# Kernel tuning notes

Hardware: AMD Instinct MI355X
Metric: run time of the kernel (lower is better)

## Reference

```python
import jax, jax.numpy as jnp
import numpy as np

DIM = 512  # module's self.dim, used for the softmax scale (note: NOT head dim)

def setup_inputs() -> dict:
    key = jax.random.key(0)
    kq, kk, kv = jax.random.split(key, 3)
    shape = (4, 8, 2048, 64)  # [B, H, S, Dh]
    q = jax.random.normal(kq, shape, dtype=jnp.float32)
    k = jax.random.normal(kk, shape, dtype=jnp.float32)
    v = jax.random.normal(kv, shape, dtype=jnp.float32)
    return {"q": q, "k": k, "v": v, "n": 2048}

def reference(q, k, v, n):
    # scores = q @ k^T, then divide by sqrt(dim) AFTER matmul (as in source)
    scores = jnp.einsum('bhqd,bhkd->bhqk', q, k)
    scale = jnp.sqrt(jnp.asarray(DIM, dtype=scores.dtype))
    p_attn = jax.nn.softmax(scores / scale, axis=-1)
    return jnp.einsum('bhqk,bhkd->bhqd', p_attn, v)
```

## Files before the change

### kernel.cpp

```cpp
#include <hip/hip_runtime.h>


using half8   = __attribute__((ext_vector_type(8))) _Float16;
using half4   = __attribute__((ext_vector_type(4))) _Float16;
using half2v  = __attribute__((ext_vector_type(2))) _Float16;
using f32x4   = __attribute__((ext_vector_type(4))) float;
using f32x16  = __attribute__((ext_vector_type(16))) float;
using int4v   = __attribute__((ext_vector_type(4))) int;

static __device__ __forceinline__ half2v cvt_pk(float a, float b) {
    return __builtin_bit_cast(half2v, __builtin_amdgcn_cvt_pkrtz(a, b));
}
static __device__ __forceinline__ int cvt_pk_i(float a, float b) {
    return __builtin_bit_cast(int, __builtin_amdgcn_cvt_pkrtz(a, b));
}

#define SEQ   2048
#define DH    64
#define QB    128
#define KVB   64
#define NKVT  (SEQ / KVB)
#define NQB   (SEQ / QB)
#define NBH   32
#define TILE_IMG_BYTES 16384
#define QSCALE (1.4426950408889634f / 22.627416997969522f)

#if __has_builtin(__builtin_amdgcn_exp2f)
#define EXP2F __builtin_amdgcn_exp2f
#else
#define EXP2F exp2f
#endif

#define GLOFF(dst, base, IMM)                                              \
    asm volatile("global_load_dwordx4 %0, %1, off offset:" #IMM            \
                 : "=v"(dst) : "v"(base) : "memory")

#define WAIT_VM(N)                                             \
    do {                                                       \
        asm volatile("s_waitcnt vmcnt(" #N ")" ::: "memory");  \
        __builtin_amdgcn_sched_barrier(0);                     \
    } while (0)

#define PLSWAP(a, b) \
    asm volatile("s_nop 1\n\tv_permlane32_swap_b32 %0, %1" : "+v"(a), "+v"(b))

#define MFMA32(A, B, C) __builtin_amdgcn_mfma_f32_32x32x16_f16((A), (B), (C), 0, 0, 0)

static __device__ __forceinline__ f32x16 z16() {
    f32x16 v;
#pragma unroll
    for (int i = 0; i < 16; ++i) v[i] = 0.f;
    return v;
}

#define ISSUE_K(KB, kvt)                                                   \
    do {                                                                   \
        const char* b0_ = imgbase + (size_t)(kvt) * TILE_IMG_BYTES + lane * 16; \
        GLOFF((KB)[0], b0_, 0);    GLOFF((KB)[1], b0_, 1024);              \
        GLOFF((KB)[2], b0_, 2048); GLOFF((KB)[3], b0_, 3072);              \
        const char* b1_ = b0_ + 4096;                                      \
        GLOFF((KB)[4], b1_, 0);    GLOFF((KB)[5], b1_, 1024);              \
        GLOFF((KB)[6], b1_, 2048); GLOFF((KB)[7], b1_, 3072);              \
    } while (0)

#define ISSUE_V(VB, kvt)                                                   \
    do {                                                                   \
        const char* b0_ = imgbase + (size_t)(kvt) * TILE_IMG_BYTES + 8192 + lane * 16; \
        GLOFF((VB)[0], b0_, 0);    GLOFF((VB)[1], b0_, 1024);              \
        GLOFF((VB)[2], b0_, 2048); GLOFF((VB)[3], b0_, 3072);              \
        const char* b1_ = b0_ + 4096;                                      \
        GLOFF((VB)[4], b1_, 0);    GLOFF((VB)[5], b1_, 1024);              \
        GLOFF((VB)[6], b1_, 2048); GLOFF((VB)[7], b1_, 3072);              \
    } while (0)

#define QK_TILE(KB, ST0, ST1)                                              \
    do {                                                                   \
        __builtin_amdgcn_s_setprio(1);                                     \
        _Pragma("unroll")                                                  \
        for (int ks = 0; ks < 4; ++ks) {                                   \
            (ST0) = MFMA32((KB)[ks],     qfrag[ks], (ST0));                \
            (ST1) = MFMA32((KB)[4 + ks], qfrag[ks], (ST1));                \
        }                                                                  \
        __builtin_amdgcn_s_setprio(0);                                     \
    } while (0)

#define SOFTPACK(ST0, ST1, PA)                                            \
    do {                                                                  \
        _Pragma("unroll")                                                 \
        for (int kvs2 = 0; kvs2 < 2; ++kvs2) {                            \
            const f32x16& st_ = kvs2 ? (ST1) : (ST0);                     \
            float p[16];                                                  \
            _Pragma("unroll")                                             \
            for (int r = 0; r < 16; ++r) p[r] = EXP2F(st_[r]);            \
            float s0 = 0.f, s1 = 0.f;                                     \
            _Pragma("unroll")                                             \
            for (int r = 0; r < 8; ++r) { s0 += p[r]; s1 += p[r + 8]; }   \
            lsum += s0 + s1;                                              \
            int m0 = cvt_pk_i(p[0],  p[1]),  m1 = cvt_pk_i(p[2],  p[3]);  \
            int m2 = cvt_pk_i(p[4],  p[5]),  m3 = cvt_pk_i(p[6],  p[7]);  \
            int m4 = cvt_pk_i(p[8],  p[9]),  m5 = cvt_pk_i(p[10], p[11]); \
            int m6 = cvt_pk_i(p[12], p[13]), m7 = cvt_pk_i(p[14], p[15]); \
            PLSWAP(m0, m2); PLSWAP(m1, m3);                               \
            PLSWAP(m4, m6); PLSWAP(m5, m7);                               \
            int4v t0; t0[0] = m0; t0[1] = m1; t0[2] = m2; t0[3] = m3;     \
            int4v t1; t1[0] = m4; t1[1] = m5; t1[2] = m6; t1[3] = m7;     \
            (PA)[2 * kvs2 + 0] = __builtin_bit_cast(half8, t0);           \
            (PA)[2 * kvs2 + 1] = __builtin_bit_cast(half8, t1);           \
        }                                                                 \
    } while (0)

#define PV_TILE(PA, VB)                                                    \
    do {                                                                   \
        __builtin_amdgcn_s_setprio(1);                                     \
        _Pragma("unroll")                                                  \
        for (int ks = 0; ks < 4; ++ks) {                                   \
            acc0 = MFMA32((PA)[ks], (VB)[ks],     acc0);                   \
            acc1 = MFMA32((PA)[ks], (VB)[4 + ks], acc1);                   \
        }                                                                  \
        __builtin_amdgcn_s_setprio(0);                                     \
    } while (0)

__global__ __launch_bounds__(256)
void prep_kv(const float* __restrict__ Kg, const float* __restrict__ Vg,
             char* __restrict__ ws)
{
    __shared__ __align__(16) _Float16 Kl[64][72];
    __shared__ __align__(16) _Float16 Vt[64][72];

    const int bid = blockIdx.x;
    const int bh  = bid >> 5;
    const int kvt = bid & 31;
    const int tid = threadIdx.x;

    const float* kg = Kg + ((size_t)bh * SEQ + (size_t)kvt * 64) * DH;
    const float* vg = Vg + ((size_t)bh * SEQ + (size_t)kvt * 64) * DH;
#pragma unroll
    for (int rr = 0; rr < 4; ++rr) {
        int row = rr * 16 + (tid >> 4);
        int c4  = (tid & 15) * 4;
        f32x4 kk = *(const f32x4*)(kg + (size_t)row * DH + c4);
        f32x4 vv = *(const f32x4*)(vg + (size_t)row * DH + c4);
#pragma unroll
        for (int j = 0; j < 4; ++j) {
            Kl[row][c4 + j] = (_Float16)kk[j];
            Vt[c4 + j][row] = (_Float16)vv[j];
        }
    }
    __syncthreads();

    char* out = ws + (size_t)bid * TILE_IMG_BYTES;
#pragma unroll
    for (int rep = 0; rep < 2; ++rep) {
        int f    = rep * 256 + tid;
        int ln   = f & 63;
        int ks   = (f >> 6) & 3;
        int g2   = f >> 8;
        int row  = g2 * 32 + (ln & 31);
        int colh = ks * 16 + (ln >> 5) * 8;
        *(half8*)(out + f * 16)        = *(const half8*)&Kl[row][colh];
        *(half8*)(out + 8192 + f * 16) = *(const half8*)&Vt[row][colh];
    }
}

__global__ __launch_bounds__(256, 2)
void fattn_fwd(const float* __restrict__ Qg, const char* __restrict__ Wimg,
               float* __restrict__ Og)
{
    const int tid  = threadIdx.x;
    const int lane = tid & 63;
    const int wave = tid >> 6;
    const int l31  = lane & 31;
    const int hi   = lane >> 5;

    const int wg  = blockIdx.x;
    const int swz = (wg & 7) * 64 + (wg >> 3);
    const int qb  = swz & (NQB - 1);
    const int bh  = swz >> 4;
    const size_t base = (size_t)bh * (SEQ * DH);

    half8 qfrag[4];
    {
        const int qrow = qb * QB + wave * 32 + l31;
        const float* qp = Qg + base + (size_t)qrow * DH + hi * 8;
#pragma unroll
        for (int ks = 0; ks < 4; ++ks) {
            f32x4 a = *(const f32x4*)(qp + ks * 16);
            f32x4 b = *(const f32x4*)(qp + ks * 16 + 4);
            half8 f;
#pragma unroll
            for (int i = 0; i < 4; ++i) f[i]     = (_Float16)(a[i] * QSCALE);
#pragma unroll
            for (int i = 0; i < 4; ++i) f[i + 4] = (_Float16)(b[i] * QSCALE);
            qfrag[ks] = f;
        }
    }

    f32x16 acc0 = z16(), acc1 = z16();
    float lsum = 0.f;

    const char* imgbase = Wimg + (size_t)(bh * NKVT) * TILE_IMG_BYTES;

    half8 kE[8], kO[8], vv[8];

    ISSUE_K(kE, 0);
    ISSUE_V(vv, 0);

#pragma unroll 1
    for (int t = 0; t < NKVT; t += 2) {
        WAIT_VM(8);
        f32x16 st0 = z16(), st1 = z16();
        QK_TILE(kE, st0, st1);
        ISSUE_K(kO, t + 1);
        half8 PA[4];
        SOFTPACK(st0, st1, PA);
        WAIT_VM(8);
        PV_TILE(PA, vv);
        ISSUE_V(vv, t + 1);

        WAIT_VM(8);
        f32x16 su0 = z16(), su1 = z16();
        QK_TILE(kO, su0, su1);
        if (t + 2 < NKVT) ISSUE_K(kE, t + 2);
        half8 PB[4];
        SOFTPACK(su0, su1, PB);
        if (t + 2 < NKVT) { WAIT_VM(8); } else { WAIT_VM(0); }
        PV_TILE(PB, vv);
        if (t + 2 < NKVT) ISSUE_V(vv, t + 2);
    }

    lsum += __shfl_xor(lsum, 32);
    const float invl = 1.f / lsum;
    const int qstrip = qb * QB + wave * 32;
#pragma unroll
    for (int r = 0; r < 16; ++r) {
        int q16 = (r & 3) + 8 * (r >> 2) + 4 * hi;
        float sc = __shfl(invl, q16);
        float* op = Og + base + (size_t)(qstrip + q16) * DH;
        op[l31]      = acc0[r] * sc;
        op[32 + l31] = acc1[r] * sc;
    }
}

extern "C" void kernel_launch(void* const* d_in, const int* in_sizes, int n_in,
                              void* d_out, int out_size, void* d_ws, size_t ws_size,
                              hipStream_t stream) {
    const float* q = (const float*)d_in[0];
    const float* k = (const float*)d_in[1];
    const float* v = (const float*)d_in[2];
    float* o = (float*)d_out;
    char* ws = (char*)d_ws;
    prep_kv<<<dim3(NBH * NKVT, 1, 1), dim3(256, 1, 1), 0, stream>>>(k, v, ws);
    fattn_fwd<<<dim3(NQB * NBH, 1, 1), dim3(256, 1, 1), 0, stream>>>(q, ws, o);
}
```

Baseline: 63.83 us.

## Stage KV tiles through shared memory via direct global-to-LDS loads

Instead of every wave loading the full K and V tile images from global memory into registers, the four waves cooperatively copy each 16KB tile into a double-buffered LDS array using global_load_lds, then each wave reads its fragments from LDS. This cuts redundant global/L2 traffic by a factor of the wave count and frees registers. In exchange it adds a workgroup barrier per KV tile, LDS read latency, and a shallower prefetch (one tile ahead, unrolled by one instead of two).

```diff
diff --git a/kernel.cpp b/kernel.cpp
--- a/kernel.cpp
+++ b/kernel.cpp
@@ -31,9 +31,10 @@
 #define EXP2F exp2f
 #endif
 
-#define GLOFF(dst, base, IMM)                                              \
-    asm volatile("global_load_dwordx4 %0, %1, off offset:" #IMM            \
-                 : "=v"(dst) : "v"(base) : "memory")
+#define GLDS(gp, lp)                                                      \
+    __builtin_amdgcn_global_load_lds(                                     \
+        (const __attribute__((address_space(1))) void*)(gp),              \
+        (__attribute__((address_space(3))) void*)(lp), 16, 0, 0)
 
 #define WAIT_VM(N)                                             \
     do {                                                       \
@@ -41,6 +42,12 @@
         __builtin_amdgcn_sched_barrier(0);                     \
     } while (0)
 
+#define WAIT_LGKM(N)                                           \
+    do {                                                       \
+        asm volatile("s_waitcnt lgkmcnt(" #N ")" ::: "memory");\
+        __builtin_amdgcn_sched_barrier(0);                     \
+    } while (0)
+
 #define PLSWAP(a, b) \
     asm volatile("s_nop 1\n\tv_permlane32_swap_b32 %0, %1" : "+v"(a), "+v"(b))
 
@@ -52,37 +59,6 @@
     for (int i = 0; i < 16; ++i) v[i] = 0.f;
     return v;
 }
-
-#define ISSUE_K(KB, kvt)                                                   \
-    do {                                                                   \
-        const char* b0_ = imgbase + (size_t)(kvt) * TILE_IMG_BYTES + lane * 16; \
-        GLOFF((KB)[0], b0_, 0);    GLOFF((KB)[1], b0_, 1024);              \
-        GLOFF((KB)[2], b0_, 2048); GLOFF((KB)[3], b0_, 3072);              \
-        const char* b1_ = b0_ + 4096;                                      \
-        GLOFF((KB)[4], b1_, 0);    GLOFF((KB)[5], b1_, 1024);              \
-        GLOFF((KB)[6], b1_, 2048); GLOFF((KB)[7], b1_, 3072);              \
-    } while (0)
-
-#define ISSUE_V(VB, kvt)                                                   \
-    do {                                                                   \
-        const char* b0_ = imgbase + (size_t)(kvt) * TILE_IMG_BYTES + 8192 + lane * 16; \
-        GLOFF((VB)[0], b0_, 0);    GLOFF((VB)[1], b0_, 1024);              \
-        GLOFF((VB)[2], b0_, 2048); GLOFF((VB)[3], b0_, 3072);              \
-        const char* b1_ = b0_ + 4096;                                      \
-        GLOFF((VB)[4], b1_, 0);    GLOFF((VB)[5], b1_, 1024);              \
-        GLOFF((VB)[6], b1_, 2048); GLOFF((VB)[7], b1_, 3072);              \
-    } while (0)
-
-#define QK_TILE(KB, ST0, ST1)                                              \
-    do {                                                                   \
-        __builtin_amdgcn_s_setprio(1);                                     \
-        _Pragma("unroll")                                                  \
-        for (int ks = 0; ks < 4; ++ks) {                                   \
-            (ST0) = MFMA32((KB)[ks],     qfrag[ks], (ST0));                \
-            (ST1) = MFMA32((KB)[4 + ks], qfrag[ks], (ST1));                \
-        }                                                                  \
-        __builtin_amdgcn_s_setprio(0);                                     \
-    } while (0)
 
 #define SOFTPACK(ST0, ST1, PA)                                            \
     do {                                                                  \
@@ -109,17 +85,6 @@
         }                                                                 \
     } while (0)
 
-#define PV_TILE(PA, VB)                                                    \
-    do {                                                                   \
-        __builtin_amdgcn_s_setprio(1);                                     \
-        _Pragma("unroll")                                                  \
-        for (int ks = 0; ks < 4; ++ks) {                                   \
-            acc0 = MFMA32((PA)[ks], (VB)[ks],     acc0);                   \
-            acc1 = MFMA32((PA)[ks], (VB)[4 + ks], acc1);                   \
-        }                                                                  \
-        __builtin_amdgcn_s_setprio(0);                                     \
-    } while (0)
-
 __global__ __launch_bounds__(256)
 void prep_kv(const float* __restrict__ Kg, const float* __restrict__ Vg,
              char* __restrict__ ws)
@@ -166,6 +131,8 @@
 void fattn_fwd(const float* __restrict__ Qg, const char* __restrict__ Wimg,
                float* __restrict__ Og)
 {
+    __shared__ __align__(16) char KVl[2][TILE_IMG_BYTES];
+
     const int tid  = threadIdx.x;
     const int lane = tid & 63;
     const int wave = tid >> 6;
@@ -199,33 +166,63 @@
     float lsum = 0.f;
 
     const char* imgbase = Wimg + (size_t)(bh * NKVT) * TILE_IMG_BYTES;
-
-    half8 kE[8], kO[8], vv[8];
-
-    ISSUE_K(kE, 0);
-    ISSUE_V(vv, 0);
+    const int sfrag = wave * 4;
+
+    auto stage = [&](int kvt, int b) {
+        const char* g = imgbase + (size_t)kvt * TILE_IMG_BYTES
+                        + sfrag * 1024 + lane * 16;
+        char* l = &KVl[b][sfrag * 1024];
+        GLDS(g,        l);
+        GLDS(g + 1024, l + 1024);
+        GLDS(g + 2048, l + 2048);
+        GLDS(g + 3072, l + 3072);
+    };
+
+    stage(0, 0);
 
 #pragma unroll 1
-    for (int t = 0; t < NKVT; t += 2) {
-        WAIT_VM(8);
+    for (int t = 0; t < NKVT; ++t) {
+        const int cur = t & 1;
+
+        WAIT_VM(0);
+        __builtin_amdgcn_s_barrier();
+        if (t + 1 < NKVT) stage(t + 1, cur ^ 1);
+
+        const char* kb = KVl[cur];
+
+        half8 kf[8];
+#pragma unroll
+        for (int j = 0; j < 8; ++j)
+            kf[j] = *(const half8*)(kb + j * 1024 + lane * 16);
+        __builtin_amdgcn_sched_barrier(0);
+        half8 vf[8];
+#pragma unroll
+        for (int j = 0; j < 8; ++j)
+            vf[j] = *(const half8*)(kb + 8192 + j * 1024 + lane * 16);
+
+        WAIT_LGKM(8);
+
         f32x16 st0 = z16(), st1 = z16();
-        QK_TILE(kE, st0, st1);
-        ISSUE_K(kO, t + 1);
+        __builtin_amdgcn_s_setprio(1);
+#pragma unroll
+        for (int ks = 0; ks < 4; ++ks) {
+            st0 = MFMA32(kf[ks],     qfrag[ks], st0);
+            st1 = MFMA32(kf[4 + ks], qfrag[ks], st1);
+        }
+        __builtin_amdgcn_s_setprio(0);
+
+        WAIT_LGKM(0);
+
         half8 PA[4];
         SOFTPACK(st0, st1, PA);
-        WAIT_VM(8);
-        PV_TILE(PA, vv);
-        ISSUE_V(vv, t + 1);
-
-        WAIT_VM(8);
-        f32x16 su0 = z16(), su1 = z16();
-        QK_TILE(kO, su0, su1);
-        if (t + 2 < NKVT) ISSUE_K(kE, t + 2);
-        half8 PB[4];
-        SOFTPACK(su0, su1, PB);
-        if (t + 2 < NKVT) { WAIT_VM(8); } else { WAIT_VM(0); }
-        PV_TILE(PB, vv);
-        if (t + 2 < NKVT) ISSUE_V(vv, t + 2);
+
+        __builtin_amdgcn_s_setprio(1);
+#pragma unroll
+        for (int ks = 0; ks < 4; ++ks) {
+            acc0 = MFMA32(PA[ks], vf[ks],     acc0);
+            acc1 = MFMA32(PA[ks], vf[4 + ks], acc1);
+        }
+        __builtin_amdgcn_s_setprio(0);
     }
 
     lsum += __shfl_xor(lsum, 32);
```

New measurement: 59.52 us. 1.07x faster.
